# Kernel tuning notes

Measured on AMD Instinct MI355X. Metric: run time of the kernel, lower is better.

The kernel has to match this reference:

```python
import jax, jax.numpy as jnp
import numpy as np

B, H, W, C = 4, 64, 64, 64
GROUPS = 32
EPS = 1e-3  # keras GroupNormalization default


def setup_inputs() -> dict:
    key = jax.random.key(0)
    ks = jax.random.split(key, 6)
    s = 1.0 / np.sqrt(C)
    return {
        'x': jax.random.normal(ks[0], (B, H, W, C), dtype=jnp.float32),
        'gamma': jnp.ones((C,), jnp.float32),
        'beta': jnp.zeros((C,), jnp.float32),
        'wq': jax.random.uniform(ks[1], (C, C), jnp.float32, -s, s),
        'bq': jnp.zeros((C,), jnp.float32),
        'wk': jax.random.uniform(ks[2], (C, C), jnp.float32, -s, s),
        'bk': jnp.zeros((C,), jnp.float32),
        'wv': jax.random.uniform(ks[3], (C, C), jnp.float32, -s, s),
        'bv': jnp.zeros((C,), jnp.float32),
        'wo': jnp.zeros((C, C), jnp.float32),  # init_scale=0.0 -> ~zero init
        'bo': jnp.zeros((C,), jnp.float32),
    }


def group_norm(x, gamma, beta):
    b, h, w, c = x.shape
    xg = x.reshape(b, h, w, GROUPS, c // GROUPS)
    mean = jnp.mean(xg, axis=(1, 2, 4), keepdims=True)
    var = jnp.var(xg, axis=(1, 2, 4), keepdims=True)
    xn = ((xg - mean) * jax.lax.rsqrt(var + EPS)).reshape(b, h, w, c)
    return xn * gamma + beta


def reference(x, gamma, beta, wq, bq, wk, bk, wv, bv, wo, bo):
    b, h, w, c = x.shape
    hn = group_norm(x, gamma, beta)
    # 1x1 convs == per-pixel dense layers
    q = jnp.einsum('bhwc,cd->bhwd', hn, wq) + bq
    k = jnp.einsum('bhwc,cd->bhwd', hn, wk) + bk
    v = jnp.einsum('bhwc,cd->bhwd', hn, wv) + bv
    # full spatial attention scores [B,H,W,H,W]
    scores = jnp.einsum('bhwc,bHWc->bhwHW', q, k) * (float(c) ** -0.5)
    attn = jax.nn.softmax(scores.reshape(b, h, w, h * w), axis=-1)
    attn = attn.reshape(b, h, w, h, w)
    o = jnp.einsum('bhwHW,bHWc->bhwc', attn, v)
    o = jnp.einsum('bhwc,cd->bhwd', o, wo) + bo
    return x + o
```

## Files before the change

kernel.cpp:

```cpp
#include <hip/hip_runtime.h>
#include <math.h>

#define BB 4
#define HH 64
#define WW 64
#define CC 64
#define NN (HH*WW)
#define NPIX (BB*NN)
#define EPS 1e-3f
#define QBLK 32
#define KSPLIT 8
#define NQT32 (NPIX/QBLK)
#define NCHK ((NN/KSPLIT)/64)

using bf16x8 = __attribute__((ext_vector_type(8))) short;
using f32x4  = __attribute__((ext_vector_type(4))) float;
using f32x16 = __attribute__((ext_vector_type(16))) float;

__device__ inline unsigned short bf16bits(float f) {
    union { float f; unsigned u; } a; a.f = f;
    unsigned r = a.u + 0x7fffu + ((a.u >> 16) & 1u);
    return (unsigned short)(r >> 16);
}
__device__ inline unsigned packbf(float lo, float hi) {
    return (unsigned)bf16bits(lo) | ((unsigned)bf16bits(hi) << 16);
}
__device__ inline unsigned cvtpk(float lo, float hi) {
    unsigned r;
    asm("v_cvt_pk_bf16_f32 %0, %1, %2" : "=v"(r) : "v"(lo), "v"(hi));
    return r;
}
#define PSWAP(a, b) asm("v_permlane32_swap_b32 %0, %1" : "+v"(a), "+v"(b))

__device__ __forceinline__ float exp2g(float x) {
    float r;
    asm("v_exp_f32 %0, %1" : "=v"(r) : "v"(x));
    return r;
}

#define QSCALE 0.18033688011112042f

__global__ __launch_bounds__(256) void gn_wt(const float* __restrict__ x,
                                             float* __restrict__ part,
                                             const float* __restrict__ wq,
                                             const float* __restrict__ wk,
                                             const float* __restrict__ wv,
                                             const float* __restrict__ wo,
                                             short* __restrict__ wfrag) {
    int t = threadIdx.x;
    if (blockIdx.x < 256) {
        int c = t & 63, rr = t >> 6;
        int p0 = blockIdx.x * 64;
        float s = 0.f, s2 = 0.f;
        #pragma unroll
        for (int k = 0; k < 16; ++k) {
            float v = x[(size_t)(p0 + rr + 4 * k) * CC + c];
            s += v; s2 += v * v;
        }
        __shared__ float sA[256], sB[256];
        sA[t] = s; sB[t] = s2;
        __syncthreads();
        if (t < 64) {
            float fs  = sA[t] + sA[64 + t] + sA[128 + t] + sA[192 + t];
            float fs2 = sB[t] + sB[64 + t] + sB[128 + t] + sB[192 + t];
            part[blockIdx.x * 128 + t]      = fs;
            part[blockIdx.x * 128 + 64 + t] = fs2;
        }
    } else {
        const float* mats[3] = {wq, wk, wv};
        int i0 = (blockIdx.x - 256) * 256 + t;
        for (int e = i0; e < 12288; e += 16 * 256) {
            int m = e >> 12;
            int r = e & 4095;
            int dt = r >> 10, h = (r >> 9) & 1, lane = (r >> 3) & 63, j = r & 7;
            int g = lane >> 4, cl = lane & 15;
            float v = mats[m][(h * 32 + g * 8 + j) * 64 + dt * 16 + cl];
            wfrag[e] = (short)bf16bits(v);
        }
        for (int e = i0; e < 4096; e += 16 * 256) {
            int j = e & 7, lane = (e >> 3) & 63, dt = (e >> 9) & 1, s = e >> 10;
            int hi = lane >> 5, l31 = lane & 31;
            float v = wo[(8 * hi + 16 * s + j) * 64 + dt * 32 + l31];
            wfrag[12288 + e] = (short)bf16bits(v);
        }
    }
}

__global__ __launch_bounds__(256) void qkv_proj(
        const float* __restrict__ x,
        const float* __restrict__ part,
        const float* __restrict__ gamma,
        const float* __restrict__ beta,
        const short* __restrict__ wfrag,
        const float* __restrict__ bq, const float* __restrict__ bk,
        const float* __restrict__ bv,
        short* __restrict__ qb, short* __restrict__ kb,
        short* __restrict__ vt) {
    __shared__ unsigned short vtile[64 * 72];
    __shared__ float sA[256], sB[256];
    __shared__ float sScale[64], sShift[64];
    int t = threadIdx.x;
    int lane = t & 63, wid = t >> 6;
    int g = lane >> 4, cl = lane & 15;
    int pixblk = blockIdx.x * 64;
    int pix0 = pixblk + wid * 16;
    int b = pixblk >> 12;

    {
        int c = t & 63, rr = t >> 6;
        float s = 0.f, s2 = 0.f;
        #pragma unroll
        for (int k = 0; k < 16; ++k) {
            int blk = b * 64 + rr + 4 * k;
            s  += part[blk * 128 + c];
            s2 += part[blk * 128 + 64 + c];
        }
        sA[t] = s; sB[t] = s2;
        __syncthreads();
        if (t < 64) {
            sA[t] = sA[t] + sA[64 + t] + sA[128 + t] + sA[192 + t];
            sB[t] = sB[t] + sB[64 + t] + sB[128 + t] + sB[192 + t];
        }
        __syncthreads();
        if (t < 64) {
            int gg = t >> 1;
            float sumg  = sA[gg * 2] + sA[gg * 2 + 1];
            float sum2g = sB[gg * 2] + sB[gg * 2 + 1];
            const float n = (float)(NN * 2);
            float mean = sumg / n;
            float var  = sum2g / n - mean * mean;
            float r = rsqrtf(var + EPS);
            float a = gamma[t] * r;
            sScale[t] = a;
            sShift[t] = beta[t] - mean * a;
        }
        __syncthreads();
    }

    const float* xp = x + (size_t)(pix0 + cl) * CC + g * 8;
    float4 x00 = *(const float4*)(xp);
    float4 x01 = *(const float4*)(xp + 4);
    float4 x10 = *(const float4*)(xp + 32);
    float4 x11 = *(const float4*)(xp + 36);
    float4 s00 = *(const float4*)(&sScale[g * 8]);
    float4 s01 = *(const float4*)(&sScale[g * 8 + 4]);
    float4 s10 = *(const float4*)(&sScale[g * 8 + 32]);
    float4 s11 = *(const float4*)(&sScale[g * 8 + 36]);
    float4 f00 = *(const float4*)(&sShift[g * 8]);
    float4 f01 = *(const float4*)(&sShift[g * 8 + 4]);
    float4 f10 = *(const float4*)(&sShift[g * 8 + 32]);
    float4 f11 = *(const float4*)(&sShift[g * 8 + 36]);

    union { bf16x8 v; unsigned u[4]; } af0, af1;
    af0.u[0] = packbf(x00.x * s00.x + f00.x, x00.y * s00.y + f00.y);
    af0.u[1] = packbf(x00.z * s00.z + f00.z, x00.w * s00.w + f00.w);
    af0.u[2] = packbf(x01.x * s01.x + f01.x, x01.y * s01.y + f01.y);
    af0.u[3] = packbf(x01.z * s01.z + f01.z, x01.w * s01.w + f01.w);
    af1.u[0] = packbf(x10.x * s10.x + f10.x, x10.y * s10.y + f10.y);
    af1.u[1] = packbf(x10.z * s10.z + f10.z, x10.w * s10.w + f10.w);
    af1.u[2] = packbf(x11.x * s11.x + f11.x, x11.y * s11.y + f11.y);
    af1.u[3] = packbf(x11.z * s11.z + f11.z, x11.w * s11.w + f11.w);

    #pragma unroll
    for (int m = 0; m < 3; ++m) {
        const float* bias = (m == 0) ? bq : (m == 1) ? bk : bv;
        #pragma unroll
        for (int dt = 0; dt < 4; ++dt) {
            bf16x8 w0 = *(const bf16x8*)(wfrag + (size_t)(((m * 4 + dt) * 2 + 0) * 64 + lane) * 8);
            bf16x8 w1 = *(const bf16x8*)(wfrag + (size_t)(((m * 4 + dt) * 2 + 1) * 64 + lane) * 8);
            f32x4 z = (f32x4){0.f, 0.f, 0.f, 0.f};
            z = __builtin_amdgcn_mfma_f32_16x16x32_bf16(af0.v, w0, z, 0, 0, 0);
            z = __builtin_amdgcn_mfma_f32_16x16x32_bf16(af1.v, w1, z, 0, 0, 0);
            float bias_d = bias[dt * 16 + cl];
            if (m == 0) {
                #pragma unroll
                for (int r = 0; r < 4; ++r)
                    qb[(size_t)(pix0 + 4 * g + r) * CC + dt * 16 + cl] =
                        (short)bf16bits((z[r] + bias_d) * QSCALE);
            } else if (m == 1) {
                #pragma unroll
                for (int r = 0; r < 4; ++r)
                    kb[(size_t)(pix0 + 4 * g + r) * CC + dt * 16 + cl] =
                        (short)bf16bits(z[r] + bias_d);
            } else {
                #pragma unroll
                for (int r = 0; r < 4; ++r)
                    vtile[(dt * 16 + cl) * 72 + wid * 16 + 4 * g + r] =
                        bf16bits(z[r] + bias_d);
            }
        }
    }
    __syncthreads();
    {
        int d = t >> 2, seg = t & 3;
        uint4 v0 = *(const uint4*)(vtile + d * 72 + seg * 16);
        uint4 v1 = *(const uint4*)(vtile + d * 72 + seg * 16 + 8);
        uint4* dst = (uint4*)(vt + ((size_t)(b * 64 + d)) * NN + pixblk + seg * 16);
        dst[0] = v0; dst[1] = v1;
    }
}

__global__ __launch_bounds__(256, 2) void attn_mfma64(
        const short* __restrict__ qb, const short* __restrict__ kb,
        const short* __restrict__ vt,
        unsigned* __restrict__ obf, float* __restrict__ msb) {
    __shared__ short lds[3][2][64 * 64];
    const int t = threadIdx.x;
    const int lane = t & 63;
    const int wid  = t >> 6;
    const int hi  = lane >> 5;
    const int l31 = lane & 31;
    const int r7  = l31 & 7;
    const int kseg   = blockIdx.x % KSPLIT;
    const int qblock = blockIdx.x / KSPLIT;
    const int qt0 = qblock * 8 + wid * 2;
    const int b = qblock >> 4;
    const int key0 = kseg * (NN / KSPLIT);

    bf16x8 qf[2][4];
    const short* qp = qb + (size_t)(qblock * 256 + wid * 64 + l31) * CC + 8 * hi;
    #pragma unroll
    for (int qc = 0; qc < 2; ++qc)
        #pragma unroll
        for (int s = 0; s < 4; ++s)
            qf[qc][s] = *(const bf16x8*)(qp + qc * 32 * CC + 16 * s);

    const int srow = t >> 3;
    const int scol = t & 7;
    const short* kS = kb + ((size_t)b * NN + key0) * CC;
    const short* vS = vt + ((size_t)b * CC) * NN + key0;

    f32x16 oacc00, oacc01, oacc10, oacc11;
    #pragma unroll
    for (int r = 0; r < 16; ++r) {
        oacc00[r] = 0.f; oacc01[r] = 0.f; oacc10[r] = 0.f; oacc11[r] = 0.f;
    }
    float psum0 = 0.f, psum1 = 0.f;

    auto stage = [&](int ck, int bsel) {
        #pragma unroll
        for (int r = 0; r < 2; ++r) {
            int row = srow + 32 * r;
            const short* src = kS + (size_t)(ck * 64 + row) * CC + (scol ^ (row & 7)) * 8;
            __builtin_amdgcn_global_load_lds(
                (const __attribute__((address_space(1))) void*)src,
                (__attribute__((address_space(3))) void*)&lds[bsel][0][(r * 32 + wid * 8) * 64],
                16, 0, 0);
        }
        #pragma unroll
        for (int r = 0; r < 2; ++r) {
            int row = srow + 32 * r;
            const short* src = vS + (size_t)row * NN + ck * 64 + (scol ^ (row & 7)) * 8;
            __builtin_amdgcn_global_load_lds(
                (const __attribute__((address_space(1))) void*)src,
                (__attribute__((address_space(3))) void*)&lds[bsel][1][(r * 32 + wid * 8) * 64],
                16, 0, 0);
        }
    };

    auto subbody = [&](const short* kB, const short* vB, int ks) {
        bf16x8 kf[4];
        #pragma unroll
        for (int s = 0; s < 4; ++s)
            kf[s] = *(const bf16x8*)(kB + (32 * ks + l31) * 64 + ((2 * s + hi) ^ r7) * 8);
        bf16x8 vf0 = *(const bf16x8*)(vB + (l31) * 64      + ((4 * ks + 0 + hi) ^ r7) * 8);
        bf16x8 vf1 = *(const bf16x8*)(vB + (32 + l31) * 64 + ((4 * ks + 0 + hi) ^ r7) * 8);
        bf16x8 vf2 = *(const bf16x8*)(vB + (l31) * 64      + ((4 * ks + 2 + hi) ^ r7) * 8);
        bf16x8 vf3 = *(const bf16x8*)(vB + (32 + l31) * 64 + ((4 * ks + 2 + hi) ^ r7) * 8);
        {
            f32x16 st;
            #pragma unroll
            for (int r = 0; r < 16; ++r) st[r] = 0.f;
            #pragma unroll
            for (int s = 0; s < 4; ++s)
                st = __builtin_amdgcn_mfma_f32_32x32x16_bf16(kf[s], qf[0][s], st, 0, 0, 0);
            float ps = 0.f;
            #pragma unroll
            for (int r = 0; r < 16; ++r) { st[r] = exp2g(st[r]); ps += st[r]; }
            psum0 += ps;
            unsigned w[8];
            #pragma unroll
            for (int i = 0; i < 8; ++i) w[i] = cvtpk(st[2 * i], st[2 * i + 1]);
            PSWAP(w[0], w[2]); PSWAP(w[1], w[3]);
            PSWAP(w[4], w[6]); PSWAP(w[5], w[7]);
            union { bf16x8 v; unsigned u[4]; } pa0, pa1;
            pa0.u[0] = w[0]; pa0.u[1] = w[1]; pa0.u[2] = w[2]; pa0.u[3] = w[3];
            pa1.u[0] = w[4]; pa1.u[1] = w[5]; pa1.u[2] = w[6]; pa1.u[3] = w[7];
            oacc00 = __builtin_amdgcn_mfma_f32_32x32x16_bf16(pa0.v, vf0, oacc00, 0, 0, 0);
            oacc01 = __builtin_amdgcn_mfma_f32_32x32x16_bf16(pa0.v, vf1, oacc01, 0, 0, 0);
            oacc00 = __builtin_amdgcn_mfma_f32_32x32x16_bf16(pa1.v, vf2, oacc00, 0, 0, 0);
            oacc01 = __builtin_amdgcn_mfma_f32_32x32x16_bf16(pa1.v, vf3, oacc01, 0, 0, 0);
        }
        {
            f32x16 st;
            #pragma unroll
            for (int r = 0; r < 16; ++r) st[r] = 0.f;
            #pragma unroll
            for (int s = 0; s < 4; ++s)
                st = __builtin_amdgcn_mfma_f32_32x32x16_bf16(kf[s], qf[1][s], st, 0, 0, 0);
            float ps = 0.f;
            #pragma unroll
            for (int r = 0; r < 16; ++r) { st[r] = exp2g(st[r]); ps += st[r]; }
            psum1 += ps;
            unsigned w[8];
            #pragma unroll
            for (int i = 0; i < 8; ++i) w[i] = cvtpk(st[2 * i], st[2 * i + 1]);
            PSWAP(w[0], w[2]); PSWAP(w[1], w[3]);
            PSWAP(w[4], w[6]); PSWAP(w[5], w[7]);
            union { bf16x8 v; unsigned u[4]; } pa0, pa1;
            pa0.u[0] = w[0]; pa0.u[1] = w[1]; pa0.u[2] = w[2]; pa0.u[3] = w[3];
            pa1.u[0] = w[4]; pa1.u[1] = w[5]; pa1.u[2] = w[6]; pa1.u[3] = w[7];
            oacc10 = __builtin_amdgcn_mfma_f32_32x32x16_bf16(pa0.v, vf0, oacc10, 0, 0, 0);
            oacc11 = __builtin_amdgcn_mfma_f32_32x32x16_bf16(pa0.v, vf1, oacc11, 0, 0, 0);
            oacc10 = __builtin_amdgcn_mfma_f32_32x32x16_bf16(pa1.v, vf2, oacc10, 0, 0, 0);
            oacc11 = __builtin_amdgcn_mfma_f32_32x32x16_bf16(pa1.v, vf3, oacc11, 0, 0, 0);
        }
    };

    stage(0, 0);
    stage(1, 1);
    #pragma unroll 1
    for (int c = 0; c < NCHK - 1; ++c) {
        asm volatile("s_waitcnt vmcnt(4)" ::: "memory");
        __builtin_amdgcn_s_barrier();
        if (c + 2 < NCHK) stage(c + 2, (c + 2) % 3);
        const short* kB = &lds[c % 3][0][0];
        const short* vB = &lds[c % 3][1][0];
        subbody(kB, vB, 0);
        subbody(kB, vB, 1);
    }
    asm volatile("s_waitcnt vmcnt(0)" ::: "memory");
    __builtin_amdgcn_s_barrier();
    {
        const int c = NCHK - 1;
        const short* kB = &lds[c % 3][0][0];
        const short* vB = &lds[c % 3][1][0];
        subbody(kB, vB, 0);
        subbody(kB, vB, 1);
    }

    {
        int task = (qt0 + 0) * KSPLIT + kseg;
        unsigned* ob32 = obf + (size_t)task * 1024;
        #pragma unroll
        for (int r = 0; r < 16; ++r) {
            int row = (r & 3) + 8 * (r >> 2) + 4 * hi;
            ob32[row * 32 + l31] = cvtpk(oacc00[r], oacc01[r]);
        }
        msb[task * 64 + lane] = psum0;
    }
    {
        int task = (qt0 + 1) * KSPLIT + kseg;
        unsigned* ob32 = obf + (size_t)task * 1024;
        #pragma unroll
        for (int r = 0; r < 16; ++r) {
            int row = (r & 3) + 8 * (r >> 2) + 4 * hi;
            ob32[row * 32 + l31] = cvtpk(oacc10[r], oacc11[r]);
        }
        msb[task * 64 + lane] = psum1;
    }
}

__device__ __forceinline__ void acc2(float& lo_acc, float& hi_acc, unsigned u) {
    union { unsigned u; float f; } a, b;
    a.u = u << 16; b.u = u & 0xffff0000u;
    lo_acc += a.f; hi_acc += b.f;
}

__global__ __launch_bounds__(256) void attn_merge_outproj(
        const unsigned* __restrict__ obf, const float* __restrict__ msb,
        const short* __restrict__ wfrag,
        const float* __restrict__ x,
        const float* __restrict__ bo,
        float* __restrict__ out) {
    int t = threadIdx.x;
    int lane = t & 63, wid = t >> 6;
    int hi = lane >> 5, l31 = lane & 31;
    int qtile = blockIdx.x * 4 + wid;

    float stot = 0.f;
    #pragma unroll
    for (int s = 0; s < KSPLIT; ++s) {
        stot += msb[(qtile * KSPLIT + s) * 64 + l31]
              + msb[(qtile * KSPLIT + s) * 64 + 32 + l31];
    }
    float inv = 1.f / stot;

    float oa[4][8];
    #pragma unroll
    for (int s = 0; s < 4; ++s)
        #pragma unroll
        for (int j = 0; j < 8; ++j) oa[s][j] = 0.f;
    #pragma unroll 4
    for (int ks = 0; ks < KSPLIT; ++ks) {
        const unsigned* base = obf + (size_t)(qtile * KSPLIT + ks) * 1024 + l31 * 32 + 8 * hi;
        uint4 wa = *(const uint4*)(base);
        uint4 wb = *(const uint4*)(base + 4);
        uint4 wc = *(const uint4*)(base + 16);
        uint4 wd = *(const uint4*)(base + 20);
        acc2(oa[0][0], oa[2][0], wa.x); acc2(oa[0][1], oa[2][1], wa.y);
        acc2(oa[0][2], oa[2][2], wa.z); acc2(oa[0][3], oa[2][3], wa.w);
        acc2(oa[0][4], oa[2][4], wb.x); acc2(oa[0][5], oa[2][5], wb.y);
        acc2(oa[0][6], oa[2][6], wb.z); acc2(oa[0][7], oa[2][7], wb.w);
        acc2(oa[1][0], oa[3][0], wc.x); acc2(oa[1][1], oa[3][1], wc.y);
        acc2(oa[1][2], oa[3][2], wc.z); acc2(oa[1][3], oa[3][3], wc.w);
        acc2(oa[1][4], oa[3][4], wd.x); acc2(oa[1][5], oa[3][5], wd.y);
        acc2(oa[1][6], oa[3][6], wd.z); acc2(oa[1][7], oa[3][7], wd.w);
    }
    union { bf16x8 v; unsigned u[4]; } af[4];
    #pragma unroll
    for (int s = 0; s < 4; ++s)
        #pragma unroll
        for (int m = 0; m < 4; ++m)
            af[s].u[m] = cvtpk(oa[s][2 * m] * inv, oa[s][2 * m + 1] * inv);

    const short* w32 = wfrag + 12288;
    f32x16 z0, z1;
    #pragma unroll
    for (int r = 0; r < 16; ++r) { z0[r] = 0.f; z1[r] = 0.f; }
    #pragma unroll
    for (int s = 0; s < 4; ++s) {
        bf16x8 wb0 = *(const bf16x8*)(w32 + (size_t)((s * 2 + 0) * 64 + lane) * 8);
        bf16x8 wb1 = *(const bf16x8*)(w32 + (size_t)((s * 2 + 1) * 64 + lane) * 8);
        z0 = __builtin_amdgcn_mfma_f32_32x32x16_bf16(af[s].v, wb0, z0, 0, 0, 0);
        z1 = __builtin_amdgcn_mfma_f32_32x32x16_bf16(af[s].v, wb1, z1, 0, 0, 0);
    }
    float bo0 = bo[l31], bo1 = bo[32 + l31];
    #pragma unroll
    for (int r = 0; r < 16; ++r) {
        int row = (r & 3) + 8 * (r >> 2) + 4 * hi;
        size_t i0 = (size_t)(qtile * QBLK + row) * CC + l31;
        out[i0]      = x[i0]      + z0[r] + bo0;
        out[i0 + 32] = x[i0 + 32] + z1[r] + bo1;
    }
}

extern "C" void kernel_launch(void* const* d_in, const int* in_sizes, int n_in,
                              void* d_out, int out_size, void* d_ws, size_t ws_size,
                              hipStream_t stream) {
    const float* x     = (const float*)d_in[0];
    const float* gamma = (const float*)d_in[1];
    const float* beta  = (const float*)d_in[2];
    const float* wq    = (const float*)d_in[3];
    const float* bq    = (const float*)d_in[4];
    const float* wk    = (const float*)d_in[5];
    const float* bk    = (const float*)d_in[6];
    const float* wv    = (const float*)d_in[7];
    const float* bv    = (const float*)d_in[8];
    const float* wo    = (const float*)d_in[9];
    const float* bo    = (const float*)d_in[10];
    float* out = (float*)d_out;

    float* ws    = (float*)d_ws;
    float* part  = ws;
    short* wfrag = (short*)(part + 32768);
    short* qb    = wfrag + 16384;
    short* kbp   = qb  + (size_t)NPIX * CC;
    short* vtp   = kbp + (size_t)NPIX * CC;
    unsigned* obf = (unsigned*)(vtp + (size_t)NPIX * CC);
    float* msb   = (float*)(obf + (size_t)NQT32 * KSPLIT * 1024);

    hipLaunchKernelGGL(gn_wt, dim3(272), dim3(256), 0, stream,
                       x, part, wq, wk, wv, wo, wfrag);
    hipLaunchKernelGGL(qkv_proj, dim3(256), dim3(256), 0, stream,
                       x, part, gamma, beta, wfrag, bq, bk, bv, qb, kbp, vtp);
    hipLaunchKernelGGL(attn_mfma64, dim3(64 * KSPLIT), dim3(256), 0, stream,
                       qb, kbp, vtp, obf, msb);
    hipLaunchKernelGGL(attn_merge_outproj, dim3(NQT32 / 4), dim3(256), 0, stream,
                       obf, msb, wfrag, x, bo, out);
}
```

Measured before the change: 45.61 us.

## Use 128-key double-buffered LDS chunks and raise MFMA wave priority

```diff
diff --git a/kernel.cpp b/kernel.cpp
--- a/kernel.cpp
+++ b/kernel.cpp
@@ -11,7 +11,8 @@
 #define QBLK 32
 #define KSPLIT 8
 #define NQT32 (NPIX/QBLK)
-#define NCHK ((NN/KSPLIT)/64)
+#define CHUNK 128
+#define NCHK ((NN/KSPLIT)/CHUNK)
 
 using bf16x8 = __attribute__((ext_vector_type(8))) short;
 using f32x4  = __attribute__((ext_vector_type(4))) float;
@@ -204,7 +205,7 @@
         const short* __restrict__ qb, const short* __restrict__ kb,
         const short* __restrict__ vt,
         unsigned* __restrict__ obf, float* __restrict__ msb) {
-    __shared__ short lds[3][2][64 * 64];
+    __shared__ short lds[2][2][128 * 64];
     const int t = threadIdx.x;
     const int lane = t & 63;
     const int wid  = t >> 6;
@@ -225,8 +226,10 @@
         for (int s = 0; s < 4; ++s)
             qf[qc][s] = *(const bf16x8*)(qp + qc * 32 * CC + 16 * s);
 
-    const int srow = t >> 3;
-    const int scol = t & 7;
+    const int srowK = t >> 3;
+    const int scolK = t & 7;
+    const int srowV = t >> 4;
+    const int scolV = t & 15;
     const short* kS = kb + ((size_t)b * NN + key0) * CC;
     const short* vS = vt + ((size_t)b * CC) * NN + key0;
 
@@ -239,41 +242,43 @@
 
     auto stage = [&](int ck, int bsel) {
         #pragma unroll
-        for (int r = 0; r < 2; ++r) {
-            int row = srow + 32 * r;
-            const short* src = kS + (size_t)(ck * 64 + row) * CC + (scol ^ (row & 7)) * 8;
+        for (int r = 0; r < 4; ++r) {
+            int row = srowK + 32 * r;
+            const short* src = kS + (size_t)(ck * CHUNK + row) * CC + (scolK ^ (row & 7)) * 8;
             __builtin_amdgcn_global_load_lds(
                 (const __attribute__((address_space(1))) void*)src,
                 (__attribute__((address_space(3))) void*)&lds[bsel][0][(r * 32 + wid * 8) * 64],
                 16, 0, 0);
         }
         #pragma unroll
-        for (int r = 0; r < 2; ++r) {
-            int row = srow + 32 * r;
-            const short* src = vS + (size_t)row * NN + ck * 64 + (scol ^ (row & 7)) * 8;
+        for (int r = 0; r < 4; ++r) {
+            int row = srowV + 16 * r;
+            const short* src = vS + (size_t)row * NN + ck * CHUNK + (scolV ^ (row & 7)) * 8;
             __builtin_amdgcn_global_load_lds(
                 (const __attribute__((address_space(1))) void*)src,
-                (__attribute__((address_space(3))) void*)&lds[bsel][1][(r * 32 + wid * 8) * 64],
+                (__attribute__((address_space(3))) void*)&lds[bsel][1][(r * 16 + wid * 4) * 128],
                 16, 0, 0);
         }
     };
 
-    auto subbody = [&](const short* kB, const short* vB, int ks) {
+    auto subbody = [&](const short* kB, const short* vB, int kst) {
         bf16x8 kf[4];
         #pragma unroll
         for (int s = 0; s < 4; ++s)
-            kf[s] = *(const bf16x8*)(kB + (32 * ks + l31) * 64 + ((2 * s + hi) ^ r7) * 8);
-        bf16x8 vf0 = *(const bf16x8*)(vB + (l31) * 64      + ((4 * ks + 0 + hi) ^ r7) * 8);
-        bf16x8 vf1 = *(const bf16x8*)(vB + (32 + l31) * 64 + ((4 * ks + 0 + hi) ^ r7) * 8);
-        bf16x8 vf2 = *(const bf16x8*)(vB + (l31) * 64      + ((4 * ks + 2 + hi) ^ r7) * 8);
-        bf16x8 vf3 = *(const bf16x8*)(vB + (32 + l31) * 64 + ((4 * ks + 2 + hi) ^ r7) * 8);
+            kf[s] = *(const bf16x8*)(kB + (32 * kst + l31) * 64 + ((2 * s + hi) ^ r7) * 8);
+        bf16x8 vf0 = *(const bf16x8*)(vB + (l31) * 128      + ((4 * kst + 0 + hi) ^ r7) * 8);
+        bf16x8 vf1 = *(const bf16x8*)(vB + (32 + l31) * 128 + ((4 * kst + 0 + hi) ^ r7) * 8);
+        bf16x8 vf2 = *(const bf16x8*)(vB + (l31) * 128      + ((4 * kst + 2 + hi) ^ r7) * 8);
+        bf16x8 vf3 = *(const bf16x8*)(vB + (32 + l31) * 128 + ((4 * kst + 2 + hi) ^ r7) * 8);
         {
             f32x16 st;
             #pragma unroll
             for (int r = 0; r < 16; ++r) st[r] = 0.f;
+            __builtin_amdgcn_s_setprio(1);
             #pragma unroll
             for (int s = 0; s < 4; ++s)
                 st = __builtin_amdgcn_mfma_f32_32x32x16_bf16(kf[s], qf[0][s], st, 0, 0, 0);
+            __builtin_amdgcn_s_setprio(0);
             float ps = 0.f;
             #pragma unroll
             for (int r = 0; r < 16; ++r) { st[r] = exp2g(st[r]); ps += st[r]; }
@@ -286,18 +291,22 @@
             union { bf16x8 v; unsigned u[4]; } pa0, pa1;
             pa0.u[0] = w[0]; pa0.u[1] = w[1]; pa0.u[2] = w[2]; pa0.u[3] = w[3];
             pa1.u[0] = w[4]; pa1.u[1] = w[5]; pa1.u[2] = w[6]; pa1.u[3] = w[7];
+            __builtin_amdgcn_s_setprio(1);
             oacc00 = __builtin_amdgcn_mfma_f32_32x32x16_bf16(pa0.v, vf0, oacc00, 0, 0, 0);
             oacc01 = __builtin_amdgcn_mfma_f32_32x32x16_bf16(pa0.v, vf1, oacc01, 0, 0, 0);
             oacc00 = __builtin_amdgcn_mfma_f32_32x32x16_bf16(pa1.v, vf2, oacc00, 0, 0, 0);
             oacc01 = __builtin_amdgcn_mfma_f32_32x32x16_bf16(pa1.v, vf3, oacc01, 0, 0, 0);
+            __builtin_amdgcn_s_setprio(0);
         }
         {
             f32x16 st;
             #pragma unroll
             for (int r = 0; r < 16; ++r) st[r] = 0.f;
+            __builtin_amdgcn_s_setprio(1);
             #pragma unroll
             for (int s = 0; s < 4; ++s)
                 st = __builtin_amdgcn_mfma_f32_32x32x16_bf16(kf[s], qf[1][s], st, 0, 0, 0);
+            __builtin_amdgcn_s_setprio(0);
             float ps = 0.f;
             #pragma unroll
             for (int r = 0; r < 16; ++r) { st[r] = exp2g(st[r]); ps += st[r]; }
@@ -310,33 +319,27 @@
             union { bf16x8 v; unsigned u[4]; } pa0, pa1;
             pa0.u[0] = w[0]; pa0.u[1] = w[1]; pa0.u[2] = w[2]; pa0.u[3] = w[3];
             pa1.u[0] = w[4]; pa1.u[1] = w[5]; pa1.u[2] = w[6]; pa1.u[3] = w[7];
+            __builtin_amdgcn_s_setprio(1);
             oacc10 = __builtin_amdgcn_mfma_f32_32x32x16_bf16(pa0.v, vf0, oacc10, 0, 0, 0);
             oacc11 = __builtin_amdgcn_mfma_f32_32x32x16_bf16(pa0.v, vf1, oacc11, 0, 0, 0);
             oacc10 = __builtin_amdgcn_mfma_f32_32x32x16_bf16(pa1.v, vf2, oacc10, 0, 0, 0);
             oacc11 = __builtin_amdgcn_mfma_f32_32x32x16_bf16(pa1.v, vf3, oacc11, 0, 0, 0);
+            __builtin_amdgcn_s_setprio(0);
         }
     };
 
     stage(0, 0);
-    stage(1, 1);
     #pragma unroll 1
-    for (int c = 0; c < NCHK - 1; ++c) {
-        asm volatile("s_waitcnt vmcnt(4)" ::: "memory");
-        __builtin_amdgcn_s_barrier();
-        if (c + 2 < NCHK) stage(c + 2, (c + 2) % 3);
-        const short* kB = &lds[c % 3][0][0];
-        const short* vB = &lds[c % 3][1][0];
+    for (int c = 0; c < NCHK; ++c) {
+        asm volatile("s_waitcnt vmcnt(0)" ::: "memory");
+        __syncthreads();
+        if (c + 1 < NCHK) stage(c + 1, (c + 1) & 1);
+        const short* kB = &lds[c & 1][0][0];
+        const short* vB = &lds[c & 1][1][0];
         subbody(kB, vB, 0);
         subbody(kB, vB, 1);
-    }
-    asm volatile("s_waitcnt vmcnt(0)" ::: "memory");
-    __builtin_amdgcn_s_barrier();
-    {
-        const int c = NCHK - 1;
-        const short* kB = &lds[c % 3][0][0];
-        const short* vB = &lds[c % 3][1][0];
-        subbody(kB, vB, 0);
-        subbody(kB, vB, 1);
+        subbody(kB, vB, 2);
+        subbody(kB, vB, 3);
     }
 
     {
```

Result: slower. 46.78 us (+2.6%).

## Use 512-thread blocks with one 32-query tile per wave in attention

Applied to the files above, without the earlier changes.

```diff
diff --git a/kernel.cpp b/kernel.cpp
--- a/kernel.cpp
+++ b/kernel.cpp
@@ -200,7 +200,7 @@
     }
 }
 
-__global__ __launch_bounds__(256, 2) void attn_mfma64(
+__global__ __launch_bounds__(512, 4) void attn_flash(
         const short* __restrict__ qb, const short* __restrict__ kb,
         const short* __restrict__ vt,
         unsigned* __restrict__ obf, float* __restrict__ msb) {
@@ -213,49 +213,36 @@
     const int r7  = l31 & 7;
     const int kseg   = blockIdx.x % KSPLIT;
     const int qblock = blockIdx.x / KSPLIT;
-    const int qt0 = qblock * 8 + wid * 2;
+    const int qtile  = qblock * 8 + wid;
     const int b = qblock >> 4;
     const int key0 = kseg * (NN / KSPLIT);
 
-    bf16x8 qf[2][4];
-    const short* qp = qb + (size_t)(qblock * 256 + wid * 64 + l31) * CC + 8 * hi;
-    #pragma unroll
-    for (int qc = 0; qc < 2; ++qc)
-        #pragma unroll
-        for (int s = 0; s < 4; ++s)
-            qf[qc][s] = *(const bf16x8*)(qp + qc * 32 * CC + 16 * s);
+    bf16x8 qf[4];
+    const short* qp = qb + (size_t)(qtile * QBLK + l31) * CC + 8 * hi;
+    #pragma unroll
+    for (int s = 0; s < 4; ++s) qf[s] = *(const bf16x8*)(qp + 16 * s);
 
     const int srow = t >> 3;
     const int scol = t & 7;
     const short* kS = kb + ((size_t)b * NN + key0) * CC;
     const short* vS = vt + ((size_t)b * CC) * NN + key0;
 
-    f32x16 oacc00, oacc01, oacc10, oacc11;
-    #pragma unroll
-    for (int r = 0; r < 16; ++r) {
-        oacc00[r] = 0.f; oacc01[r] = 0.f; oacc10[r] = 0.f; oacc11[r] = 0.f;
-    }
-    float psum0 = 0.f, psum1 = 0.f;
+    f32x16 oacc0, oacc1;
+    #pragma unroll
+    for (int r = 0; r < 16; ++r) { oacc0[r] = 0.f; oacc1[r] = 0.f; }
+    float psum = 0.f;
 
     auto stage = [&](int ck, int bsel) {
-        #pragma unroll
-        for (int r = 0; r < 2; ++r) {
-            int row = srow + 32 * r;
-            const short* src = kS + (size_t)(ck * 64 + row) * CC + (scol ^ (row & 7)) * 8;
-            __builtin_amdgcn_global_load_lds(
-                (const __attribute__((address_space(1))) void*)src,
-                (__attribute__((address_space(3))) void*)&lds[bsel][0][(r * 32 + wid * 8) * 64],
-                16, 0, 0);
-        }
-        #pragma unroll
-        for (int r = 0; r < 2; ++r) {
-            int row = srow + 32 * r;
-            const short* src = vS + (size_t)row * NN + ck * 64 + (scol ^ (row & 7)) * 8;
-            __builtin_amdgcn_global_load_lds(
-                (const __attribute__((address_space(1))) void*)src,
-                (__attribute__((address_space(3))) void*)&lds[bsel][1][(r * 32 + wid * 8) * 64],
-                16, 0, 0);
-        }
+        const short* srcK = kS + (size_t)(ck * 64 + srow) * CC + (scol ^ (srow & 7)) * 8;
+        __builtin_amdgcn_global_load_lds(
+            (const __attribute__((address_space(1))) void*)srcK,
+            (__attribute__((address_space(3))) void*)&lds[bsel][0][wid * 512],
+            16, 0, 0);
+        const short* srcV = vS + (size_t)srow * NN + ck * 64 + (scol ^ (srow & 7)) * 8;
+        __builtin_amdgcn_global_load_lds(
+            (const __attribute__((address_space(1))) void*)srcV,
+            (__attribute__((address_space(3))) void*)&lds[bsel][1][wid * 512],
+            16, 0, 0);
     };
 
     auto subbody = [&](const short* kB, const short* vB, int ks) {
@@ -267,61 +254,35 @@
         bf16x8 vf1 = *(const bf16x8*)(vB + (32 + l31) * 64 + ((4 * ks + 0 + hi) ^ r7) * 8);
         bf16x8 vf2 = *(const bf16x8*)(vB + (l31) * 64      + ((4 * ks + 2 + hi) ^ r7) * 8);
         bf16x8 vf3 = *(const bf16x8*)(vB + (32 + l31) * 64 + ((4 * ks + 2 + hi) ^ r7) * 8);
-        {
-            f32x16 st;
-            #pragma unroll
-            for (int r = 0; r < 16; ++r) st[r] = 0.f;
-            #pragma unroll
-            for (int s = 0; s < 4; ++s)
-                st = __builtin_amdgcn_mfma_f32_32x32x16_bf16(kf[s], qf[0][s], st, 0, 0, 0);
-            float ps = 0.f;
-            #pragma unroll
-            for (int r = 0; r < 16; ++r) { st[r] = exp2g(st[r]); ps += st[r]; }
-            psum0 += ps;
-            unsigned w[8];
-            #pragma unroll
-            for (int i = 0; i < 8; ++i) w[i] = cvtpk(st[2 * i], st[2 * i + 1]);
-            PSWAP(w[0], w[2]); PSWAP(w[1], w[3]);
-            PSWAP(w[4], w[6]); PSWAP(w[5], w[7]);
-            union { bf16x8 v; unsigned u[4]; } pa0, pa1;
-            pa0.u[0] = w[0]; pa0.u[1] = w[1]; pa0.u[2] = w[2]; pa0.u[3] = w[3];
-            pa1.u[0] = w[4]; pa1.u[1] = w[5]; pa1.u[2] = w[6]; pa1.u[3] = w[7];
-            oacc00 = __builtin_amdgcn_mfma_f32_32x32x16_bf16(pa0.v, vf0, oacc00, 0, 0, 0);
-            oacc01 = __builtin_amdgcn_mfma_f32_32x32x16_bf16(pa0.v, vf1, oacc01, 0, 0, 0);
-            oacc00 = __builtin_amdgcn_mfma_f32_32x32x16_bf16(pa1.v, vf2, oacc00, 0, 0, 0);
-            oacc01 = __builtin_amdgcn_mfma_f32_32x32x16_bf16(pa1.v, vf3, oacc01, 0, 0, 0);
-        }
-        {
-            f32x16 st;
-            #pragma unroll
-            for (int r = 0; r < 16; ++r) st[r] = 0.f;
-            #pragma unroll
-            for (int s = 0; s < 4; ++s)
-                st = __builtin_amdgcn_mfma_f32_32x32x16_bf16(kf[s], qf[1][s], st, 0, 0, 0);
-            float ps = 0.f;
-            #pragma unroll
-            for (int r = 0; r < 16; ++r) { st[r] = exp2g(st[r]); ps += st[r]; }
-            psum1 += ps;
-            unsigned w[8];
-            #pragma unroll
-            for (int i = 0; i < 8; ++i) w[i] = cvtpk(st[2 * i], st[2 * i + 1]);
-            PSWAP(w[0], w[2]); PSWAP(w[1], w[3]);
-            PSWAP(w[4], w[6]); PSWAP(w[5], w[7]);
-            union { bf16x8 v; unsigned u[4]; } pa0, pa1;
-            pa0.u[0] = w[0]; pa0.u[1] = w[1]; pa0.u[2] = w[2]; pa0.u[3] = w[3];
-            pa1.u[0] = w[4]; pa1.u[1] = w[5]; pa1.u[2] = w[6]; pa1.u[3] = w[7];
-            oacc10 = __builtin_amdgcn_mfma_f32_32x32x16_bf16(pa0.v, vf0, oacc10, 0, 0, 0);
-            oacc11 = __builtin_amdgcn_mfma_f32_32x32x16_bf16(pa0.v, vf1, oacc11, 0, 0, 0);
-            oacc10 = __builtin_amdgcn_mfma_f32_32x32x16_bf16(pa1.v, vf2, oacc10, 0, 0, 0);
-            oacc11 = __builtin_amdgcn_mfma_f32_32x32x16_bf16(pa1.v, vf3, oacc11, 0, 0, 0);
-        }
+        f32x16 st;
+        #pragma unroll
+        for (int r = 0; r < 16; ++r) st[r] = 0.f;
+        #pragma unroll
+        for (int s = 0; s < 4; ++s)
+            st = __builtin_amdgcn_mfma_f32_32x32x16_bf16(kf[s], qf[s], st, 0, 0, 0);
+        float ps = 0.f;
+        #pragma unroll
+        for (int r = 0; r < 16; ++r) { st[r] = exp2g(st[r]); ps += st[r]; }
+        psum += ps;
+        unsigned w[8];
+        #pragma unroll
+        for (int i = 0; i < 8; ++i) w[i] = cvtpk(st[2 * i], st[2 * i + 1]);
+        PSWAP(w[0], w[2]); PSWAP(w[1], w[3]);
+        PSWAP(w[4], w[6]); PSWAP(w[5], w[7]);
+        union { bf16x8 v; unsigned u[4]; } pa0, pa1;
+        pa0.u[0] = w[0]; pa0.u[1] = w[1]; pa0.u[2] = w[2]; pa0.u[3] = w[3];
+        pa1.u[0] = w[4]; pa1.u[1] = w[5]; pa1.u[2] = w[6]; pa1.u[3] = w[7];
+        oacc0 = __builtin_amdgcn_mfma_f32_32x32x16_bf16(pa0.v, vf0, oacc0, 0, 0, 0);
+        oacc1 = __builtin_amdgcn_mfma_f32_32x32x16_bf16(pa0.v, vf1, oacc1, 0, 0, 0);
+        oacc0 = __builtin_amdgcn_mfma_f32_32x32x16_bf16(pa1.v, vf2, oacc0, 0, 0, 0);
+        oacc1 = __builtin_amdgcn_mfma_f32_32x32x16_bf16(pa1.v, vf3, oacc1, 0, 0, 0);
     };
 
     stage(0, 0);
     stage(1, 1);
     #pragma unroll 1
     for (int c = 0; c < NCHK - 1; ++c) {
-        asm volatile("s_waitcnt vmcnt(4)" ::: "memory");
+        asm volatile("s_waitcnt vmcnt(2)" ::: "memory");
         __builtin_amdgcn_s_barrier();
         if (c + 2 < NCHK) stage(c + 2, (c + 2) % 3);
         const short* kB = &lds[c % 3][0][0];
@@ -339,26 +300,14 @@
         subbody(kB, vB, 1);
     }
 
-    {
-        int task = (qt0 + 0) * KSPLIT + kseg;
-        unsigned* ob32 = obf + (size_t)task * 1024;
-        #pragma unroll
-        for (int r = 0; r < 16; ++r) {
-            int row = (r & 3) + 8 * (r >> 2) + 4 * hi;
-            ob32[row * 32 + l31] = cvtpk(oacc00[r], oacc01[r]);
-        }
-        msb[task * 64 + lane] = psum0;
-    }
-    {
-        int task = (qt0 + 1) * KSPLIT + kseg;
-        unsigned* ob32 = obf + (size_t)task * 1024;
-        #pragma unroll
-        for (int r = 0; r < 16; ++r) {
-            int row = (r & 3) + 8 * (r >> 2) + 4 * hi;
-            ob32[row * 32 + l31] = cvtpk(oacc10[r], oacc11[r]);
-        }
-        msb[task * 64 + lane] = psum1;
-    }
+    int task = qtile * KSPLIT + kseg;
+    unsigned* ob32 = obf + (size_t)task * 1024;
+    #pragma unroll
+    for (int r = 0; r < 16; ++r) {
+        int row = (r & 3) + 8 * (r >> 2) + 4 * hi;
+        ob32[row * 32 + l31] = cvtpk(oacc0[r], oacc1[r]);
+    }
+    msb[task * 64 + lane] = psum;
 }
 
 __device__ __forceinline__ void acc2(float& lo_acc, float& hi_acc, unsigned u) {
@@ -464,7 +413,7 @@
                        x, part, wq, wk, wv, wo, wfrag);
     hipLaunchKernelGGL(qkv_proj, dim3(256), dim3(256), 0, stream,
                        x, part, gamma, beta, wfrag, bq, bk, bv, qb, kbp, vtp);
-    hipLaunchKernelGGL(attn_mfma64, dim3(64 * KSPLIT), dim3(256), 0, stream,
+    hipLaunchKernelGGL(attn_flash, dim3(64 * KSPLIT), dim3(512), 0, stream,
                        qb, kbp, vtp, obf, msb);
     hipLaunchKernelGGL(attn_merge_outproj, dim3(NQT32 / 4), dim3(256), 0, stream,
                        obf, msb, wfrag, x, bo, out);
```

After: 45.60 us. About the same (-0.0%).
